# Kernel tuning notes

Measured on AMD Instinct MI355X. Metric: run time of the kernel, lower is better.

## Reference

```python
import jax, jax.numpy as jnp
import numpy as np

N_USER = 100_000
N_ITEM = 100_000
E = 1_600_000
D_IN = 128
H = 64
OUT = 2


def _lin_init(k, din, dout):
    kw, kb = jax.random.split(k)
    bound = 1.0 / np.sqrt(din)
    W = jax.random.uniform(kw, (din, dout), jnp.float32, -bound, bound)
    b = jax.random.uniform(kb, (dout,), jnp.float32, -bound, bound)
    return W, b


def setup_inputs() -> dict:
    key = jax.random.key(0)
    ks = jax.random.split(key, 12)
    inp = {
        "x_user": jax.random.normal(ks[0], (N_USER, D_IN), jnp.float32),
        "x_item": jax.random.normal(ks[1], (N_ITEM, D_IN), jnp.float32),
        "ei_user": jax.random.randint(ks[2], (2, E), 0, N_USER, jnp.int32),
        "ei_item": jax.random.randint(ks[3], (2, E), 0, N_ITEM, jnp.int32),
    }
    inp["W1_user"], inp["b1_user"] = _lin_init(ks[4], D_IN, H)
    inp["W1_item"], inp["b1_item"] = _lin_init(ks[5], D_IN, H)
    inp["W2_user"], inp["b2_user"] = _lin_init(ks[6], H, H)
    inp["W2_item"], inp["b2_item"] = _lin_init(ks[7], H, H)
    inp["Wl_user"], inp["bl_user"] = _lin_init(ks[8], H, OUT)
    inp["Wl_item"], inp["bl_item"] = _lin_init(ks[9], H, OUT)
    return inp


def gcn_conv(x, W, b, src, dst, n):
    # PyG GCNConv: h = x @ W; symmetric norm with added self-loops; scatter-add to dst; + bias
    loop = jnp.arange(n, dtype=src.dtype)
    s = jnp.concatenate([src, loop])  # [E+n]
    d = jnp.concatenate([dst, loop])
    deg = jax.ops.segment_sum(jnp.ones(s.shape[0], x.dtype), d, num_segments=n)
    dinv = jnp.where(deg > 0, jax.lax.rsqrt(deg), 0.0)
    norm = dinv[s] * dinv[d]  # [E+n]
    h = x @ W  # [n, out]
    msg = h[s] * norm[:, None]  # gather + scale, [E+n, out]
    return jax.ops.segment_sum(msg, d, num_segments=n) + b


def reference(x_user, x_item, ei_user, ei_item,
              W1_user, b1_user, W1_item, b1_item,
              W2_user, b2_user, W2_item, b2_item,
              Wl_user, bl_user, Wl_item, bl_item):
    # layer 1 (HeteroConv with one GCNConv per node type's relation) + relu; dropout = identity (eval)
    h_u = jax.nn.relu(gcn_conv(x_user, W1_user, b1_user, ei_user[0], ei_user[1], N_USER))
    h_i = jax.nn.relu(gcn_conv(x_item, W1_item, b1_item, ei_item[0], ei_item[1], N_ITEM))
    # layer 2 + relu
    h_u = jax.nn.relu(gcn_conv(h_u, W2_user, b2_user, ei_user[0], ei_user[1], N_USER))
    h_i = jax.nn.relu(gcn_conv(h_i, W2_item, b2_item, ei_item[0], ei_item[1], N_ITEM))
    # per-node-type output heads
    return (h_u @ Wl_user + bl_user, h_i @ Wl_item + bl_item)
```

## Files before the change

### kernel.cpp

```cpp
#include <hip/hip_runtime.h>

#define CDIV(a,b) (((a)+(b)-1)/(b))
#define NPB 256
#define PCHUNK 2048

typedef __attribute__((ext_vector_type(8))) short bf16x8;
typedef __attribute__((ext_vector_type(8))) unsigned short u16x8;
typedef __attribute__((ext_vector_type(4))) float f32x4;

__device__ __forceinline__ unsigned short f2bf(float x){
    unsigned int u = __float_as_uint(x);
    unsigned int r = u + 0x7FFFu + ((u >> 16) & 1u);
    return (unsigned short)(r >> 16);
}
__device__ __forceinline__ float bf2f(unsigned short h){
    return __uint_as_float(((unsigned int)h) << 16);
}

__global__ __launch_bounds__(256) void hg_wsplit_all(const float* __restrict__ W1u, const float* __restrict__ W1i,
                                                     const float* __restrict__ W2u, const float* __restrict__ W2i,
                                                     unsigned short* __restrict__ Bhi, unsigned short* __restrict__ Blo){
    const int sid = blockIdx.x*256 + threadIdx.x;
    if (sid >= 3072) return;
    const float* W; int slot, base;
    if (sid < 1024)      { W = W1u; slot = sid;        base = 0;     }
    else if (sid < 2048) { W = W1i; slot = sid - 1024; base = 8192;  }
    else if (sid < 2560) { W = W2u; slot = sid - 2048; base = 16384; }
    else                 { W = W2i; slot = sid - 2560; base = 20480; }
    const int l  = slot & 63;
    const int ct = (slot >> 6) & 3;
    const int ks = slot >> 8;
    const int kb = ks*32 + (l >> 4)*8;
    const int c  = ct*16 + (l & 15);
    #pragma unroll
    for (int j = 0; j < 8; ++j){
        const float w = W[(size_t)(kb + j)*64 + c];
        const unsigned short h = f2bf(w);
        Bhi[(size_t)base + (size_t)slot*8 + j] = h;
        Blo[(size_t)base + (size_t)slot*8 + j] = f2bf(w - bf2f(h));
    }
}

__device__ __forceinline__ void gemm1_body(int gb,
                                           const float* __restrict__ XU, const float* __restrict__ XI,
                                           const unsigned short* __restrict__ Bhi, const unsigned short* __restrict__ Blo,
                                           unsigned short* __restrict__ GU, unsigned short* __restrict__ GI,
                                           int NU, int NI, int gbU){
    const int type = (gb >= gbU);
    const int blk  = type ? gb - gbU : gb;
    const float* X = type ? XI : XU;
    unsigned short* G = type ? GI : GU;
    const int N    = type ? NI : NU;
    const unsigned short* Bh = Bhi + (type ? 8192 : 0);
    const unsigned short* Bl = Blo + (type ? 8192 : 0);

    const int l = threadIdx.x & 63;
    const int w = threadIdx.x >> 6;
    const int row0 = blk*64 + w*16;
    if (row0 >= N) return;

    f32x4 acc[4];
    #pragma unroll
    for (int ct = 0; ct < 4; ++ct) acc[ct] = (f32x4){0.f,0.f,0.f,0.f};

    const int rA = row0 + (l & 15);
    const int kg = (l >> 4) * 8;
    const bool rowok = (rA < N);
    const float* xrow = X + (size_t)rA * 128;

    #pragma unroll
    for (int ks = 0; ks < 4; ++ks){
        float xv[8];
        if (rowok){
            const float4 a = *(const float4*)(xrow + ks*32 + kg);
            const float4 b = *(const float4*)(xrow + ks*32 + kg + 4);
            xv[0]=a.x; xv[1]=a.y; xv[2]=a.z; xv[3]=a.w;
            xv[4]=b.x; xv[5]=b.y; xv[6]=b.z; xv[7]=b.w;
        } else {
            #pragma unroll
            for (int j = 0; j < 8; ++j) xv[j] = 0.f;
        }
        bf16x8 ahi, alo;
        #pragma unroll
        for (int j = 0; j < 8; ++j){
            const unsigned short h = f2bf(xv[j]);
            ahi[j] = (short)h;
            alo[j] = (short)f2bf(xv[j] - bf2f(h));
        }
        #pragma unroll
        for (int ct = 0; ct < 4; ++ct){
            const bf16x8 bhi = *(const bf16x8*)(Bh + ((size_t)(ks*4 + ct)*64 + l)*8);
            const bf16x8 blo = *(const bf16x8*)(Bl + ((size_t)(ks*4 + ct)*64 + l)*8);
            acc[ct] = __builtin_amdgcn_mfma_f32_16x16x32_bf16(ahi, bhi, acc[ct], 0, 0, 0);
            acc[ct] = __builtin_amdgcn_mfma_f32_16x16x32_bf16(alo, bhi, acc[ct], 0, 0, 0);
            acc[ct] = __builtin_amdgcn_mfma_f32_16x16x32_bf16(ahi, blo, acc[ct], 0, 0, 0);
        }
    }

    const int orow0 = row0 + (l >> 4)*4;
    const int ocol  = l & 15;
    #pragma unroll
    for (int r = 0; r < 4; ++r){
        const int orow = orow0 + r;
        if (orow < N){
            #pragma unroll
            for (int ct = 0; ct < 4; ++ct)
                G[(size_t)orow*64 + ct*16 + ocol] = f2bf(acc[ct][r]);
        }
    }
}

#define GEMM_TAIL(taskTot) \
    if ((int)blockIdx.x >= (taskTot)){ \
        gemm1_body(goff + blockIdx.x - (taskTot), XU, XI, Bhi, Blo, GU, GI, NU, NI, gbU); \
        return; \
    }

__global__ __launch_bounds__(256) void hg_mega_chist(const int* __restrict__ eiU, const int* __restrict__ eiI,
                                                     int* __restrict__ chU, int* __restrict__ chI,
                                                     int EU, int EI, int pbU, int pbTot, int NB,
                                                     const float* __restrict__ XU, const float* __restrict__ XI,
                                                     const unsigned short* __restrict__ Bhi, const unsigned short* __restrict__ Blo,
                                                     unsigned short* __restrict__ GU, unsigned short* __restrict__ GI,
                                                     int NU, int NI, int gbU, int goff){
    GEMM_TAIL(pbTot)
    extern __shared__ int sh[];
    const int type = ((int)blockIdx.x >= pbU);
    const int blk  = type ? blockIdx.x - pbU : blockIdx.x;
    const int E    = type ? EI : EU;
    const int* dst = (type ? eiI : eiU) + E;
    int* chist     = (type ? chI : chU) + (size_t)blk * NB;
    for (int i = threadIdx.x; i < NB; i += 256) sh[i] = 0;
    __syncthreads();
    const int e0 = blk * PCHUNK;
    const int eend = min(e0 + PCHUNK, E);
    for (int e = e0 + threadIdx.x; e < eend; e += 256)
        atomicAdd(&sh[dst[e] >> 8], 1);
    __syncthreads();
    for (int i = threadIdx.x; i < NB; i += 256)
        chist[i] = sh[i];
}

__global__ __launch_bounds__(256) void hg_mega_colscan(int* __restrict__ chU, int* __restrict__ chI,
                                                       int* __restrict__ bhU, int* __restrict__ bhI,
                                                       int pbU, int pbI, int NB,
                                                       const float* __restrict__ XU, const float* __restrict__ XI,
                                                       const unsigned short* __restrict__ Bhi, const unsigned short* __restrict__ Blo,
                                                       unsigned short* __restrict__ GU, unsigned short* __restrict__ GI,
                                                       int NU, int NI, int gbU, int goff){
    GEMM_TAIL(2*NB)
    __shared__ int sc[256];
    const int type = ((int)blockIdx.x >= NB);
    const int b    = type ? blockIdx.x - NB : blockIdx.x;
    int* chist     = type ? chI : chU;
    int* bh        = type ? bhI : bhU;
    const int nch  = type ? pbI : pbU;
    const int t = threadIdx.x;
    int carry = 0;
    for (int seg = 0; seg < nch; seg += 256){
        const int idx = seg + t;
        const int v = (idx < nch) ? chist[(size_t)idx*NB + b] : 0;
        sc[t] = v;
        __syncthreads();
        for (int off = 1; off < 256; off <<= 1){
            int x = 0;
            if (t >= off) x = sc[t-off];
            __syncthreads();
            if (t >= off) sc[t] += x;
            __syncthreads();
        }
        if (idx < nch) chist[(size_t)idx*NB + b] = carry + sc[t] - v;
        const int tot = sc[255];
        __syncthreads();
        carry += tot;
    }
    if (t == 0) bh[b] = carry;
}

__global__ __launch_bounds__(256) void hg_mega_bscan(const int* __restrict__ bhU, const int* __restrict__ bhI,
                                                     int* __restrict__ boffU, int* __restrict__ boffI,
                                                     int NB, int EU, int EI,
                                                     const float* __restrict__ XU, const float* __restrict__ XI,
                                                     const unsigned short* __restrict__ Bhi, const unsigned short* __restrict__ Blo,
                                                     unsigned short* __restrict__ GU, unsigned short* __restrict__ GI,
                                                     int NU, int NI, int gbU, int goff){
    GEMM_TAIL(2)
    __shared__ int sc[256];
    const int type = blockIdx.x;
    const int* bh = type ? bhI : bhU;
    int* boff     = type ? boffI : boffU;
    const int E   = type ? EI : EU;
    const int t = threadIdx.x;
    const int i0 = 2*t, i1 = 2*t + 1;
    const int c0 = (i0 < NB) ? bh[i0] : 0;
    const int c1 = (i1 < NB) ? bh[i1] : 0;
    const int s = c0 + c1;
    sc[t] = s;
    __syncthreads();
    for (int off = 1; off < 256; off <<= 1){
        int x = 0;
        if (t >= off) x = sc[t-off];
        __syncthreads();
        if (t >= off) sc[t] += x;
        __syncthreads();
    }
    const int excl = sc[t] - s;
    if (i0 < NB) boff[i0] = excl;
    if (i1 < NB) boff[i1] = excl + c0;
    if (t == 0) boff[NB] = E;
}

__global__ __launch_bounds__(256) void hg_mega_part(const int* __restrict__ eiU, const int* __restrict__ eiI,
                                                    const int* __restrict__ chU, const int* __restrict__ chI,
                                                    const int* __restrict__ boffU, const int* __restrict__ boffI,
                                                    unsigned int* __restrict__ bkU, unsigned int* __restrict__ bkI,
                                                    int EU, int EI, int pbU, int pbTot, int NB,
                                                    const float* __restrict__ XU, const float* __restrict__ XI,
                                                    const unsigned short* __restrict__ Bhi, const unsigned short* __restrict__ Blo,
                                                    unsigned short* __restrict__ GU, unsigned short* __restrict__ GI,
                                                    int NU, int NI, int gbU, int goff){
    GEMM_TAIL(pbTot)
    extern __shared__ int sh[];
    int* lofs  = sh;
    int* lcur  = lofs + NB;
    int* lbase = lcur + NB;
    int* sc    = lbase + NB;
    unsigned int* stage = (unsigned int*)(sc + 256);
    int* gaddr = (int*)(stage + PCHUNK);

    const int type = ((int)blockIdx.x >= pbU);
    const int blk  = type ? blockIdx.x - pbU : blockIdx.x;
    const int E    = type ? EI : EU;
    const int* src = type ? eiI : eiU;
    const int* dst = src + E;
    const int* chist = (type ? chI : chU) + (size_t)blk * NB;
    const int* boff  = type ? boffI : boffU;
    unsigned int* bucketed = type ? bkI : bkU;

    const int t  = threadIdx.x;
    const int e0 = blk * PCHUNK;
    const int eend = min(e0 + PCHUNK, E);
    const int cnt  = eend - e0;

    int se[8], de[8];
    for (int i = t; i < NB; i += 256) lofs[i] = 0;
    __syncthreads();
    const int eb = e0 + t*8;
    if (eb + 8 <= E){
        const int4 sa = *(const int4*)(src + eb);
        const int4 sb = *(const int4*)(src + eb + 4);
        const int4 da = *(const int4*)(dst + eb);
        const int4 db = *(const int4*)(dst + eb + 4);
        se[0]=sa.x; se[1]=sa.y; se[2]=sa.z; se[3]=sa.w;
        se[4]=sb.x; se[5]=sb.y; se[6]=sb.z; se[7]=sb.w;
        de[0]=da.x; de[1]=da.y; de[2]=da.z; de[3]=da.w;
        de[4]=db.x; de[5]=db.y; de[6]=db.z; de[7]=db.w;
    } else {
        #pragma unroll
        for (int j = 0; j < 8; ++j){
            const int e = eb + j;
            se[j] = (e < E) ? src[e] : -1;
            de[j] = (e < E) ? dst[e] : -1;
        }
    }
    #pragma unroll
    for (int j = 0; j < 8; ++j)
        if (de[j] >= 0) atomicAdd(&lofs[de[j] >> 8], 1);
    __syncthreads();

    const int i0 = 2*t, i1 = 2*t + 1;
    const int c0 = (i0 < NB) ? lofs[i0] : 0;
    const int c1 = (i1 < NB) ? lofs[i1] : 0;
    if (i0 < NB) lbase[i0] = boff[i0] + chist[i0];
    if (i1 < NB) lbase[i1] = boff[i1] + chist[i1];
    const int s = c0 + c1;
    sc[t] = s;
    __syncthreads();
    for (int off = 1; off < 256; off <<= 1){
        int x = 0;
        if (t >= off) x = sc[t-off];
        __syncthreads();
        if (t >= off) sc[t] += x;
        __syncthreads();
    }
    const int excl = sc[t] - s;
    __syncthreads();
    if (i0 < NB){ lofs[i0] = excl;      lcur[i0] = excl; }
    if (i1 < NB){ lofs[i1] = excl + c0; lcur[i1] = excl + c0; }
    __syncthreads();

    #pragma unroll
    for (int j = 0; j < 8; ++j){
        if (de[j] >= 0){
            const int b = de[j] >> 8;
            const int p = atomicAdd(&lcur[b], 1);
            stage[p] = (unsigned int)se[j] | ((unsigned int)(de[j] & 255) << 24);
            gaddr[p] = lbase[b] + (p - lofs[b]);
        }
    }
    __syncthreads();

    for (int i = t; i < cnt; i += 256)
        bucketed[gaddr[i]] = stage[i];
}

__global__ __launch_bounds__(256) void hg_mega_build(const unsigned int* __restrict__ bkU, const unsigned int* __restrict__ bkI,
                                                     const int* __restrict__ boffU, const int* __restrict__ boffI,
                                                     float* __restrict__ dinvU, float* __restrict__ dinvI,
                                                     int* __restrict__ rowptrU, int* __restrict__ rowptrI,
                                                     int* __restrict__ csrU, int* __restrict__ csrI,
                                                     int NU, int NI, int EU, int EI, int nbU, int nbTot,
                                                     const float* __restrict__ XU, const float* __restrict__ XI,
                                                     const unsigned short* __restrict__ Bhi, const unsigned short* __restrict__ Blo,
                                                     unsigned short* __restrict__ GU, unsigned short* __restrict__ GI,
                                                     int gbU, int goff){
    GEMM_TAIL(nbTot)
    __shared__ int hist[NPB];
    __shared__ int sc[NPB];
    __shared__ int cur[NPB];
    const int type = ((int)blockIdx.x >= nbU);
    const int b    = type ? blockIdx.x - nbU : blockIdx.x;
    const unsigned int* bucketed = type ? bkI : bkU;
    const int* boff = type ? boffI : boffU;
    float* dinv     = type ? dinvI : dinvU;
    int* rowptr     = type ? rowptrI : rowptrU;
    int* csr_src    = type ? csrI : csrU;
    const int N     = type ? NI : NU;
    const int E     = type ? EI : EU;

    const int t   = threadIdx.x;
    const int beg = boff[b], end = boff[b+1];
    hist[t] = 0;
    __syncthreads();
    for (int i = beg + t; i < end; i += 256)
        atomicAdd(&hist[bucketed[i] >> 24], 1);
    __syncthreads();
    const int d = hist[t];
    sc[t] = d;
    __syncthreads();
    for (int off = 1; off < 256; off <<= 1){
        int x = 0;
        if (t >= off) x = sc[t-off];
        __syncthreads();
        if (t >= off) sc[t] += x;
        __syncthreads();
    }
    const int excl = sc[t] - d;
    const int v = b*NPB + t;
    if (v < N){
        dinv[v]   = rsqrtf((float)(d + 1));
        rowptr[v] = beg + excl;
    }
    if (b == 0 && t == 0) rowptr[N] = E;
    cur[t] = beg + excl;
    __syncthreads();
    for (int i = beg + t; i < end; i += 256){
        const unsigned int w = bucketed[i];
        const int p = atomicAdd(&cur[w >> 24], 1);
        csr_src[p] = (int)(w & 0x00FFFFFFu);
    }
}

__global__ __launch_bounds__(256) void hg_gemm2(const float* __restrict__ XU, const float* __restrict__ XI,
                                                const unsigned short* __restrict__ Bhi, const unsigned short* __restrict__ Blo,
                                                unsigned short* __restrict__ GU, unsigned short* __restrict__ GI,
                                                int NU, int NI, int gbU){
    const int type = ((int)blockIdx.x >= gbU);
    const int blk  = type ? blockIdx.x - gbU : blockIdx.x;
    const float* X = type ? XI : XU;
    unsigned short* G = type ? GI : GU;
    const int N    = type ? NI : NU;
    const unsigned short* Bh = Bhi + (type ? 20480 : 16384);
    const unsigned short* Bl = Blo + (type ? 20480 : 16384);

    const int l = threadIdx.x & 63;
    const int w = threadIdx.x >> 6;
    const int row0 = blk*64 + w*16;
    if (row0 >= N) return;

    f32x4 acc[4];
    #pragma unroll
    for (int ct = 0; ct < 4; ++ct) acc[ct] = (f32x4){0.f,0.f,0.f,0.f};

    const int rA = row0 + (l & 15);
    const int kg = (l >> 4) * 8;
    const bool rowok = (rA < N);
    const float* xrow = X + (size_t)rA * 64;

    #pragma unroll
    for (int ks = 0; ks < 2; ++ks){
        float xv[8];
        if (rowok){
            const float4 a = *(const float4*)(xrow + ks*32 + kg);
            const float4 b = *(const float4*)(xrow + ks*32 + kg + 4);
            xv[0]=a.x; xv[1]=a.y; xv[2]=a.z; xv[3]=a.w;
            xv[4]=b.x; xv[5]=b.y; xv[6]=b.z; xv[7]=b.w;
        } else {
            #pragma unroll
            for (int j = 0; j < 8; ++j) xv[j] = 0.f;
        }
        bf16x8 ahi, alo;
        #pragma unroll
        for (int j = 0; j < 8; ++j){
            const unsigned short h = f2bf(xv[j]);
            ahi[j] = (short)h;
            alo[j] = (short)f2bf(xv[j] - bf2f(h));
        }
        #pragma unroll
        for (int ct = 0; ct < 4; ++ct){
            const bf16x8 bhi = *(const bf16x8*)(Bh + ((size_t)(ks*4 + ct)*64 + l)*8);
            const bf16x8 blo = *(const bf16x8*)(Bl + ((size_t)(ks*4 + ct)*64 + l)*8);
            acc[ct] = __builtin_amdgcn_mfma_f32_16x16x32_bf16(ahi, bhi, acc[ct], 0, 0, 0);
            acc[ct] = __builtin_amdgcn_mfma_f32_16x16x32_bf16(alo, bhi, acc[ct], 0, 0, 0);
            acc[ct] = __builtin_amdgcn_mfma_f32_16x16x32_bf16(ahi, blo, acc[ct], 0, 0, 0);
        }
    }

    const int orow0 = row0 + (l >> 4)*4;
    const int ocol  = l & 15;
    #pragma unroll
    for (int r = 0; r < 4; ++r){
        const int orow = orow0 + r;
        if (orow < N){
            #pragma unroll
            for (int ct = 0; ct < 4; ++ct)
                G[(size_t)orow*64 + ct*16 + ocol] = f2bf(acc[ct][r]);
        }
    }
}

template<bool HEAD>
__device__ __forceinline__ void agg_body(const unsigned short* __restrict__ g,
                                         const int* __restrict__ csr_src, const int* __restrict__ rowptr,
                                         const float* __restrict__ dinv, const float* __restrict__ b,
                                         const float* __restrict__ Wl, const float* __restrict__ bl,
                                         float* __restrict__ outp, int blk, int N){
    const int wave = (blk*256 + (int)threadIdx.x) >> 6;
    const int sub  = (threadIdx.x >> 3) & 7;
    const int c8   = (threadIdx.x & 7) << 3;
    const int v    = wave*8 + sub;
    const bool ok  = (v < N);

    int beg = 0, cnt = 0;
    float dvv = 0.f;
    if (ok){ beg = rowptr[v]; cnt = rowptr[v+1] - beg; dvv = dinv[v]; }

    float acc[8];
    #pragma unroll
    for (int j = 0; j < 8; ++j) acc[j] = 0.f;
    if (ok){
        const u16x8 s = *(const u16x8*)(g + (size_t)v*64 + c8);
        #pragma unroll
        for (int j = 0; j < 8; ++j) acc[j] = bf2f(s[j]) * dvv;
    }

    int i = 0;
    for (; i + 8 <= cnt; i += 8){
        const int s0 = csr_src[beg+i+0]; const int s1 = csr_src[beg+i+1];
        const int s2 = csr_src[beg+i+2]; const int s3 = csr_src[beg+i+3];
        const int s4 = csr_src[beg+i+4]; const int s5 = csr_src[beg+i+5];
        const int s6 = csr_src[beg+i+6]; const int s7 = csr_src[beg+i+7];
        const float dv0 = dinv[s0]; const float dv1 = dinv[s1];
        const float dv2 = dinv[s2]; const float dv3 = dinv[s3];
        const float dv4 = dinv[s4]; const float dv5 = dinv[s5];
        const float dv6 = dinv[s6]; const float dv7 = dinv[s7];
        const u16x8 x0 = *(const u16x8*)(g + (size_t)s0*64 + c8);
        const u16x8 x1 = *(const u16x8*)(g + (size_t)s1*64 + c8);
        const u16x8 x2 = *(const u16x8*)(g + (size_t)s2*64 + c8);
        const u16x8 x3 = *(const u16x8*)(g + (size_t)s3*64 + c8);
        const u16x8 x4 = *(const u16x8*)(g + (size_t)s4*64 + c8);
        const u16x8 x5 = *(const u16x8*)(g + (size_t)s5*64 + c8);
        const u16x8 x6 = *(const u16x8*)(g + (size_t)s6*64 + c8);
        const u16x8 x7 = *(const u16x8*)(g + (size_t)s7*64 + c8);
        #pragma unroll
        for (int j = 0; j < 8; ++j){
            float a = fmaf(bf2f(x0[j]), dv0, fmaf(bf2f(x1[j]), dv1, fmaf(bf2f(x2[j]), dv2, bf2f(x3[j]) * dv3)));
            float c = fmaf(bf2f(x4[j]), dv4, fmaf(bf2f(x5[j]), dv5, fmaf(bf2f(x6[j]), dv6, bf2f(x7[j]) * dv7)));
            acc[j] += a + c;
        }
    }
    for (; i + 4 <= cnt; i += 4){
        const int s0 = csr_src[beg+i+0]; const int s1 = csr_src[beg+i+1];
        const int s2 = csr_src[beg+i+2]; const int s3 = csr_src[beg+i+3];
        const float dv0 = dinv[s0]; const float dv1 = dinv[s1];
        const float dv2 = dinv[s2]; const float dv3 = dinv[s3];
        const u16x8 x0 = *(const u16x8*)(g + (size_t)s0*64 + c8);
        const u16x8 x1 = *(const u16x8*)(g + (size_t)s1*64 + c8);
        const u16x8 x2 = *(const u16x8*)(g + (size_t)s2*64 + c8);
        const u16x8 x3 = *(const u16x8*)(g + (size_t)s3*64 + c8);
        #pragma unroll
        for (int j = 0; j < 8; ++j)
            acc[j] += fmaf(bf2f(x0[j]), dv0, fmaf(bf2f(x1[j]), dv1, fmaf(bf2f(x2[j]), dv2, bf2f(x3[j]) * dv3)));
    }
    for (; i < cnt; ++i){
        const int s0 = csr_src[beg+i];
        const float dv0 = dinv[s0];
        const u16x8 x0 = *(const u16x8*)(g + (size_t)s0*64 + c8);
        #pragma unroll
        for (int j = 0; j < 8; ++j) acc[j] = fmaf(bf2f(x0[j]), dv0, acc[j]);
    }

    float r[8];
    {
        const float4 b0 = *(const float4*)(b + c8);
        const float4 b1 = *(const float4*)(b + c8 + 4);
        r[0] = fmaxf(fmaf(acc[0], dvv, b0.x), 0.f);
        r[1] = fmaxf(fmaf(acc[1], dvv, b0.y), 0.f);
        r[2] = fmaxf(fmaf(acc[2], dvv, b0.z), 0.f);
        r[3] = fmaxf(fmaf(acc[3], dvv, b0.w), 0.f);
        r[4] = fmaxf(fmaf(acc[4], dvv, b1.x), 0.f);
        r[5] = fmaxf(fmaf(acc[5], dvv, b1.y), 0.f);
        r[6] = fmaxf(fmaf(acc[6], dvv, b1.z), 0.f);
        r[7] = fmaxf(fmaf(acc[7], dvv, b1.w), 0.f);
    }

    if (!HEAD){
        if (ok){
            float4 r0 = {r[0], r[1], r[2], r[3]};
            float4 r1 = {r[4], r[5], r[6], r[7]};
            *(float4*)(outp + (size_t)v*64 + c8)     = r0;
            *(float4*)(outp + (size_t)v*64 + c8 + 4) = r1;
        }
    } else {
        float p0 = 0.f, p1 = 0.f;
        #pragma unroll
        for (int j = 0; j < 8; ++j){
            const float2 wl = *(const float2*)(Wl + (size_t)(c8 + j)*2);
            p0 = fmaf(r[j], wl.x, p0);
            p1 = fmaf(r[j], wl.y, p1);
        }
        p0 += __shfl_xor(p0, 1); p1 += __shfl_xor(p1, 1);
        p0 += __shfl_xor(p0, 2); p1 += __shfl_xor(p1, 2);
        p0 += __shfl_xor(p0, 4); p1 += __shfl_xor(p1, 4);
        if (ok && (threadIdx.x & 7) == 0){
            float2 o; o.x = p0 + bl[0]; o.y = p1 + bl[1];
            *(float2*)(outp + (size_t)v*2) = o;
        }
    }
}

__global__ __launch_bounds__(256) void hg_aggregate3(const unsigned short* __restrict__ gU, const unsigned short* __restrict__ gI,
                                                     const int* __restrict__ csrU, const int* __restrict__ csrI,
                                                     const int* __restrict__ rowptrU, const int* __restrict__ rowptrI,
                                                     const float* __restrict__ dinvU, const float* __restrict__ dinvI,
                                                     const float* __restrict__ bU, const float* __restrict__ bI,
                                                     float* __restrict__ outU, float* __restrict__ outI,
                                                     int NU, int NI, int nbU){
    const int type = ((int)blockIdx.x >= nbU);
    const int blk  = type ? blockIdx.x - nbU : blockIdx.x;
    agg_body<false>(type ? gI : gU, type ? csrI : csrU, type ? rowptrI : rowptrU,
                    type ? dinvI : dinvU, type ? bI : bU, nullptr, nullptr,
                    type ? outI : outU, blk, type ? NI : NU);
}

__global__ __launch_bounds__(256) void hg_agghead(const unsigned short* __restrict__ gU, const unsigned short* __restrict__ gI,
                                                  const int* __restrict__ csrU, const int* __restrict__ csrI,
                                                  const int* __restrict__ rowptrU, const int* __restrict__ rowptrI,
                                                  const float* __restrict__ dinvU, const float* __restrict__ dinvI,
                                                  const float* __restrict__ bU, const float* __restrict__ bI,
                                                  const float* __restrict__ WlU, const float* __restrict__ WlI,
                                                  const float* __restrict__ blU, const float* __restrict__ blI,
                                                  float* __restrict__ outU, float* __restrict__ outI,
                                                  int NU, int NI, int nbU){
    const int type = ((int)blockIdx.x >= nbU);
    const int blk  = type ? blockIdx.x - nbU : blockIdx.x;
    agg_body<true>(type ? gI : gU, type ? csrI : csrU, type ? rowptrI : rowptrU,
                   type ? dinvI : dinvU, type ? bI : bU,
                   type ? WlI : WlU, type ? blI : blU,
                   type ? outI : outU, blk, type ? NI : NU);
}

extern "C" void kernel_launch(void* const* d_in, const int* in_sizes, int n_in,
                              void* d_out, int out_size, void* d_ws, size_t ws_size,
                              hipStream_t stream) {
    const float* x_user = (const float*)d_in[0];
    const float* x_item = (const float*)d_in[1];
    const int*  ei_user = (const int*)d_in[2];
    const int*  ei_item = (const int*)d_in[3];
    const float* W1_user = (const float*)d_in[4];
    const float* b1_user = (const float*)d_in[5];
    const float* W1_item = (const float*)d_in[6];
    const float* b1_item = (const float*)d_in[7];
    const float* W2_user = (const float*)d_in[8];
    const float* b2_user = (const float*)d_in[9];
    const float* W2_item = (const float*)d_in[10];
    const float* b2_item = (const float*)d_in[11];
    const float* Wl_user = (const float*)d_in[12];
    const float* bl_user = (const float*)d_in[13];
    const float* Wl_item = (const float*)d_in[14];
    const float* bl_item = (const float*)d_in[15];

    const int NU = in_sizes[0] / 128;
    const int NI = in_sizes[1] / 128;
    const int EU = in_sizes[2] / 2;
    const int EI = in_sizes[3] / 2;
    const int NBU = CDIV(NU, NPB);
    const int NBI = CDIV(NI, NPB);
    const int NB  = (NBU > NBI) ? NBU : NBI;
    const int pbU = CDIV(EU, PCHUNK), pbI = CDIV(EI, PCHUNK);

    char* w = (char*)d_ws;
    float* hFU = (float*)w;                     w += (size_t)NU * 64 * sizeof(float);
    float* hFI = (float*)w;                     w += (size_t)NI * 64 * sizeof(float);
    unsigned short* GU = (unsigned short*)w;    w += (size_t)NU * 64 * sizeof(unsigned short);
    unsigned short* GI = (unsigned short*)w;    w += (size_t)NI * 64 * sizeof(unsigned short);
    float* dinvU = (float*)w;                   w += (size_t)NU * sizeof(float);
    float* dinvI = (float*)w;                   w += (size_t)NI * sizeof(float);
    int* rowptrU = (int*)w;                     w += ((size_t)NU + 1) * sizeof(int);
    int* rowptrI = (int*)w;                     w += ((size_t)NI + 1) * sizeof(int);
    int* csrU = (int*)w;                        w += (size_t)EU * sizeof(int);
    int* csrI = (int*)w;                        w += (size_t)EI * sizeof(int);
    unsigned int* bkU = (unsigned int*)w;       w += (size_t)EU * sizeof(int);
    unsigned int* bkI = (unsigned int*)w;       w += (size_t)EI * sizeof(int);
    int* chU = (int*)w;                         w += (size_t)pbU * NB * sizeof(int);
    int* chI = (int*)w;                         w += (size_t)pbI * NB * sizeof(int);
    int* bhU = (int*)w;                         w += (size_t)NB * sizeof(int);
    int* bhI = (int*)w;                         w += (size_t)NB * sizeof(int);
    int* boffU = (int*)w;                       w += ((size_t)NB + 1) * sizeof(int);
    int* boffI = (int*)w;                       w += ((size_t)NB + 1) * sizeof(int);
    unsigned short* Bhi = (unsigned short*)w;   w += (size_t)24576 * sizeof(unsigned short);
    unsigned short* Blo = (unsigned short*)w;   w += (size_t)24576 * sizeof(unsigned short);

    float* out  = (float*)d_out;
    float* outU = out;
    float* outI = out + (size_t)2 * NU;

    const int gbU = CDIV(NU, 64), gbI = CDIV(NI, 64);
    const int GB = gbU + gbI;
    const int q = GB / 5;
    const int c1 = q, c2 = q, c3 = q, c4 = q, c5 = GB - 4*q;

    hg_wsplit_all<<<12, 256, 0, stream>>>(W1_user, W1_item, W2_user, W2_item, Bhi, Blo);

    hg_mega_chist<<<pbU + pbI + c1, 256, NB*sizeof(int), stream>>>(
        ei_user, ei_item, chU, chI, EU, EI, pbU, pbU + pbI, NB,
        x_user, x_item, Bhi, Blo, GU, GI, NU, NI, gbU, 0);
    hg_mega_colscan<<<2*NB + c2, 256, 0, stream>>>(
        chU, chI, bhU, bhI, pbU, pbI, NB,
        x_user, x_item, Bhi, Blo, GU, GI, NU, NI, gbU, c1);
    hg_mega_bscan<<<2 + c3, 256, 0, stream>>>(
        bhU, bhI, boffU, boffI, NB, EU, EI,
        x_user, x_item, Bhi, Blo, GU, GI, NU, NI, gbU, c1 + c2);
    const size_t p5lds = (size_t)(3*NB + 256 + 2*PCHUNK) * sizeof(int);
    hg_mega_part<<<pbU + pbI + c4, 256, p5lds, stream>>>(
        ei_user, ei_item, chU, chI, boffU, boffI, bkU, bkI, EU, EI, pbU, pbU + pbI, NB,
        x_user, x_item, Bhi, Blo, GU, GI, NU, NI, gbU, c1 + c2 + c3);
    hg_mega_build<<<NBU + NBI + c5, 256, 0, stream>>>(
        bkU, bkI, boffU, boffI, dinvU, dinvI, rowptrU, rowptrI, csrU, csrI,
        NU, NI, EU, EI, NBU, NBU + NBI,
        x_user, x_item, Bhi, Blo, GU, GI, gbU, c1 + c2 + c3 + c4);

    const int abU = CDIV(NU, 32), abI = CDIV(NI, 32);
    hg_aggregate3<<<abU + abI, 256, 0, stream>>>(GU, GI, csrU, csrI, rowptrU, rowptrI,
                                                 dinvU, dinvI, b1_user, b1_item, hFU, hFI, NU, NI, abU);

    hg_gemm2<<<gbU + gbI, 256, 0, stream>>>(hFU, hFI, Bhi, Blo, GU, GI, NU, NI, gbU);

    hg_agghead<<<abU + abI, 256, 0, stream>>>(GU, GI, csrU, csrI, rowptrU, rowptrI,
                                              dinvU, dinvI, b2_user, b2_item,
                                              Wl_user, Wl_item, bl_user, bl_item,
                                              outU, outI, NU, NI, abU);
}
```

Measured before the change: 256.2 us.

## Fuse layer-1 aggregation with layer-2 GEMM through shared memory

```diff
diff --git a/kernel.cpp b/kernel.cpp
--- a/kernel.cpp
+++ b/kernel.cpp
@@ -361,91 +361,14 @@
     }
 }
 
-__global__ __launch_bounds__(256) void hg_gemm2(const float* __restrict__ XU, const float* __restrict__ XI,
-                                                const unsigned short* __restrict__ Bhi, const unsigned short* __restrict__ Blo,
-                                                unsigned short* __restrict__ GU, unsigned short* __restrict__ GI,
-                                                int NU, int NI, int gbU){
-    const int type = ((int)blockIdx.x >= gbU);
-    const int blk  = type ? blockIdx.x - gbU : blockIdx.x;
-    const float* X = type ? XI : XU;
-    unsigned short* G = type ? GI : GU;
-    const int N    = type ? NI : NU;
-    const unsigned short* Bh = Bhi + (type ? 20480 : 16384);
-    const unsigned short* Bl = Blo + (type ? 20480 : 16384);
-
-    const int l = threadIdx.x & 63;
-    const int w = threadIdx.x >> 6;
-    const int row0 = blk*64 + w*16;
-    if (row0 >= N) return;
-
-    f32x4 acc[4];
-    #pragma unroll
-    for (int ct = 0; ct < 4; ++ct) acc[ct] = (f32x4){0.f,0.f,0.f,0.f};
-
-    const int rA = row0 + (l & 15);
-    const int kg = (l >> 4) * 8;
-    const bool rowok = (rA < N);
-    const float* xrow = X + (size_t)rA * 64;
-
-    #pragma unroll
-    for (int ks = 0; ks < 2; ++ks){
-        float xv[8];
-        if (rowok){
-            const float4 a = *(const float4*)(xrow + ks*32 + kg);
-            const float4 b = *(const float4*)(xrow + ks*32 + kg + 4);
-            xv[0]=a.x; xv[1]=a.y; xv[2]=a.z; xv[3]=a.w;
-            xv[4]=b.x; xv[5]=b.y; xv[6]=b.z; xv[7]=b.w;
-        } else {
-            #pragma unroll
-            for (int j = 0; j < 8; ++j) xv[j] = 0.f;
-        }
-        bf16x8 ahi, alo;
-        #pragma unroll
-        for (int j = 0; j < 8; ++j){
-            const unsigned short h = f2bf(xv[j]);
-            ahi[j] = (short)h;
-            alo[j] = (short)f2bf(xv[j] - bf2f(h));
-        }
-        #pragma unroll
-        for (int ct = 0; ct < 4; ++ct){
-            const bf16x8 bhi = *(const bf16x8*)(Bh + ((size_t)(ks*4 + ct)*64 + l)*8);
-            const bf16x8 blo = *(const bf16x8*)(Bl + ((size_t)(ks*4 + ct)*64 + l)*8);
-            acc[ct] = __builtin_amdgcn_mfma_f32_16x16x32_bf16(ahi, bhi, acc[ct], 0, 0, 0);
-            acc[ct] = __builtin_amdgcn_mfma_f32_16x16x32_bf16(alo, bhi, acc[ct], 0, 0, 0);
-            acc[ct] = __builtin_amdgcn_mfma_f32_16x16x32_bf16(ahi, blo, acc[ct], 0, 0, 0);
-        }
-    }
-
-    const int orow0 = row0 + (l >> 4)*4;
-    const int ocol  = l & 15;
-    #pragma unroll
-    for (int r = 0; r < 4; ++r){
-        const int orow = orow0 + r;
-        if (orow < N){
-            #pragma unroll
-            for (int ct = 0; ct < 4; ++ct)
-                G[(size_t)orow*64 + ct*16 + ocol] = f2bf(acc[ct][r]);
-        }
-    }
-}
-
-template<bool HEAD>
-__device__ __forceinline__ void agg_body(const unsigned short* __restrict__ g,
-                                         const int* __restrict__ csr_src, const int* __restrict__ rowptr,
-                                         const float* __restrict__ dinv, const float* __restrict__ b,
-                                         const float* __restrict__ Wl, const float* __restrict__ bl,
-                                         float* __restrict__ outp, int blk, int N){
-    const int wave = (blk*256 + (int)threadIdx.x) >> 6;
-    const int sub  = (threadIdx.x >> 3) & 7;
-    const int c8   = (threadIdx.x & 7) << 3;
-    const int v    = wave*8 + sub;
-    const bool ok  = (v < N);
-
+__device__ __forceinline__ void gather_core(const unsigned short* __restrict__ g,
+                                            const int* __restrict__ csr_src, const int* __restrict__ rowptr,
+                                            const float* __restrict__ dinv, int v, int c8, bool ok,
+                                            float* acc, float& dvv){
     int beg = 0, cnt = 0;
-    float dvv = 0.f;
+    dvv = 0.f;
     if (ok){ beg = rowptr[v]; cnt = rowptr[v+1] - beg; dvv = dinv[v]; }
 
-    float acc[8];
     #pragma unroll
     for (int j = 0; j < 8; ++j) acc[j] = 0.f;
     if (ok){
@@ -499,6 +422,131 @@
         #pragma unroll
         for (int j = 0; j < 8; ++j) acc[j] = fmaf(bf2f(x0[j]), dv0, acc[j]);
     }
+}
+
+__global__ __launch_bounds__(256) void hg_agg_gemm2(const unsigned short* __restrict__ gU, const unsigned short* __restrict__ gI,
+                                                    const int* __restrict__ csrU, const int* __restrict__ csrI,
+                                                    const int* __restrict__ rowptrU, const int* __restrict__ rowptrI,
+                                                    const float* __restrict__ dinvU, const float* __restrict__ dinvI,
+                                                    const float* __restrict__ bU, const float* __restrict__ bI,
+                                                    const unsigned short* __restrict__ Bhi, const unsigned short* __restrict__ Blo,
+                                                    unsigned short* __restrict__ G2U, unsigned short* __restrict__ G2I,
+                                                    int NU, int NI, int nbU){
+    __shared__ float hrow[32*68];
+    const int type = ((int)blockIdx.x >= nbU);
+    const int blk  = type ? blockIdx.x - nbU : blockIdx.x;
+    const unsigned short* g = type ? gI : gU;
+    const int* csr_src = type ? csrI : csrU;
+    const int* rowptr  = type ? rowptrI : rowptrU;
+    const float* dinv  = type ? dinvI : dinvU;
+    const float* b     = type ? bI : bU;
+    unsigned short* G2 = type ? G2I : G2U;
+    const int N        = type ? NI : NU;
+    const unsigned short* Bh = Bhi + (type ? 20480 : 16384);
+    const unsigned short* Bl = Blo + (type ? 20480 : 16384);
+
+    const int t = threadIdx.x;
+    const int nodeLocal = t >> 3;
+    const int c8 = (t & 7) << 3;
+    const int v = blk*32 + nodeLocal;
+    const bool ok = (v < N);
+
+    float acc[8]; float dvv;
+    gather_core(g, csr_src, rowptr, dinv, v, c8, ok, acc, dvv);
+
+    {
+        const float4 b0 = *(const float4*)(b + c8);
+        const float4 b1 = *(const float4*)(b + c8 + 4);
+        float r0 = ok ? fmaxf(fmaf(acc[0], dvv, b0.x), 0.f) : 0.f;
+        float r1 = ok ? fmaxf(fmaf(acc[1], dvv, b0.y), 0.f) : 0.f;
+        float r2 = ok ? fmaxf(fmaf(acc[2], dvv, b0.z), 0.f) : 0.f;
+        float r3 = ok ? fmaxf(fmaf(acc[3], dvv, b0.w), 0.f) : 0.f;
+        float r4 = ok ? fmaxf(fmaf(acc[4], dvv, b1.x), 0.f) : 0.f;
+        float r5 = ok ? fmaxf(fmaf(acc[5], dvv, b1.y), 0.f) : 0.f;
+        float r6 = ok ? fmaxf(fmaf(acc[6], dvv, b1.z), 0.f) : 0.f;
+        float r7 = ok ? fmaxf(fmaf(acc[7], dvv, b1.w), 0.f) : 0.f;
+        float* hr = hrow + nodeLocal*68 + c8;
+        hr[0]=r0; hr[1]=r1; hr[2]=r2; hr[3]=r3; hr[4]=r4; hr[5]=r5; hr[6]=r6; hr[7]=r7;
+    }
+    __syncthreads();
+
+    const int l  = t & 63;
+    const int wv = t >> 6;
+    const int rbase  = (wv & 1) * 16;
+    const int ctbase = (wv >> 1) * 2;
+
+    f32x4 acc2[2];
+    acc2[0] = (f32x4){0.f,0.f,0.f,0.f};
+    acc2[1] = (f32x4){0.f,0.f,0.f,0.f};
+
+    const int arow = rbase + (l & 15);
+    const int kg   = (l >> 4) * 8;
+    #pragma unroll
+    for (int ks = 0; ks < 2; ++ks){
+        const float* hr = hrow + arow*68 + ks*32 + kg;
+        const float4 a = *(const float4*)(hr);
+        const float4 c = *(const float4*)(hr + 4);
+        float xv[8] = {a.x,a.y,a.z,a.w,c.x,c.y,c.z,c.w};
+        bf16x8 ahi, alo;
+        #pragma unroll
+        for (int j = 0; j < 8; ++j){
+            const unsigned short h = f2bf(xv[j]);
+            ahi[j] = (short)h;
+            alo[j] = (short)f2bf(xv[j] - bf2f(h));
+        }
+        #pragma unroll
+        for (int ct = 0; ct < 2; ++ct){
+            const int slot = (ks*4 + ctbase + ct)*64 + l;
+            const bf16x8 bhi = *(const bf16x8*)(Bh + (size_t)slot*8);
+            const bf16x8 blo = *(const bf16x8*)(Bl + (size_t)slot*8);
+            acc2[ct] = __builtin_amdgcn_mfma_f32_16x16x32_bf16(ahi, bhi, acc2[ct], 0, 0, 0);
+            acc2[ct] = __builtin_amdgcn_mfma_f32_16x16x32_bf16(alo, bhi, acc2[ct], 0, 0, 0);
+            acc2[ct] = __builtin_amdgcn_mfma_f32_16x16x32_bf16(ahi, blo, acc2[ct], 0, 0, 0);
+        }
+    }
+
+    const int orow0 = rbase + (l >> 4)*4;
+    const int ocol  = l & 15;
+    #pragma unroll
+    for (int r = 0; r < 4; ++r){
+        const int gv = blk*32 + orow0 + r;
+        if (gv < N){
+            #pragma unroll
+            for (int ct = 0; ct < 2; ++ct)
+                G2[(size_t)gv*64 + (ctbase + ct)*16 + ocol] = f2bf(acc2[ct][r]);
+        }
+    }
+}
+
+__global__ __launch_bounds__(256) void hg_agghead(const unsigned short* __restrict__ gU, const unsigned short* __restrict__ gI,
+                                                  const int* __restrict__ csrU, const int* __restrict__ csrI,
+                                                  const int* __restrict__ rowptrU, const int* __restrict__ rowptrI,
+                                                  const float* __restrict__ dinvU, const float* __restrict__ dinvI,
+                                                  const float* __restrict__ bU, const float* __restrict__ bI,
+                                                  const float* __restrict__ WlU, const float* __restrict__ WlI,
+                                                  const float* __restrict__ blU, const float* __restrict__ blI,
+                                                  float* __restrict__ outU, float* __restrict__ outI,
+                                                  int NU, int NI, int nbU){
+    const int type = ((int)blockIdx.x >= nbU);
+    const int blk  = type ? blockIdx.x - nbU : blockIdx.x;
+    const unsigned short* g = type ? gI : gU;
+    const int* csr_src = type ? csrI : csrU;
+    const int* rowptr  = type ? rowptrI : rowptrU;
+    const float* dinv  = type ? dinvI : dinvU;
+    const float* b     = type ? bI : bU;
+    const float* Wl    = type ? WlI : WlU;
+    const float* bl    = type ? blI : blU;
+    float* outp        = type ? outI : outU;
+    const int N        = type ? NI : NU;
+
+    const int t = threadIdx.x;
+    const int nodeLocal = t >> 3;
+    const int c8 = (t & 7) << 3;
+    const int v = blk*32 + nodeLocal;
+    const bool ok = (v < N);
+
+    float acc[8]; float dvv;
+    gather_core(g, csr_src, rowptr, dinv, v, c8, ok, acc, dvv);
 
     float r[8];
     {
@@ -514,60 +562,20 @@
         r[7] = fmaxf(fmaf(acc[7], dvv, b1.w), 0.f);
     }
 
-    if (!HEAD){
-        if (ok){
-            float4 r0 = {r[0], r[1], r[2], r[3]};
-            float4 r1 = {r[4], r[5], r[6], r[7]};
-            *(float4*)(outp + (size_t)v*64 + c8)     = r0;
-            *(float4*)(outp + (size_t)v*64 + c8 + 4) = r1;
-        }
-    } else {
-        float p0 = 0.f, p1 = 0.f;
-        #pragma unroll
-        for (int j = 0; j < 8; ++j){
-            const float2 wl = *(const float2*)(Wl + (size_t)(c8 + j)*2);
-            p0 = fmaf(r[j], wl.x, p0);
-            p1 = fmaf(r[j], wl.y, p1);
-        }
-        p0 += __shfl_xor(p0, 1); p1 += __shfl_xor(p1, 1);
-        p0 += __shfl_xor(p0, 2); p1 += __shfl_xor(p1, 2);
-        p0 += __shfl_xor(p0, 4); p1 += __shfl_xor(p1, 4);
-        if (ok && (threadIdx.x & 7) == 0){
-            float2 o; o.x = p0 + bl[0]; o.y = p1 + bl[1];
-            *(float2*)(outp + (size_t)v*2) = o;
-        }
-    }
-}
-
-__global__ __launch_bounds__(256) void hg_aggregate3(const unsigned short* __restrict__ gU, const unsigned short* __restrict__ gI,
-                                                     const int* __restrict__ csrU, const int* __restrict__ csrI,
-                                                     const int* __restrict__ rowptrU, const int* __restrict__ rowptrI,
-                                                     const float* __restrict__ dinvU, const float* __restrict__ dinvI,
-                                                     const float* __restrict__ bU, const float* __restrict__ bI,
-                                                     float* __restrict__ outU, float* __restrict__ outI,
-                                                     int NU, int NI, int nbU){
-    const int type = ((int)blockIdx.x >= nbU);
-    const int blk  = type ? blockIdx.x - nbU : blockIdx.x;
-    agg_body<false>(type ? gI : gU, type ? csrI : csrU, type ? rowptrI : rowptrU,
-                    type ? dinvI : dinvU, type ? bI : bU, nullptr, nullptr,
-                    type ? outI : outU, blk, type ? NI : NU);
-}
-
-__global__ __launch_bounds__(256) void hg_agghead(const unsigned short* __restrict__ gU, const unsigned short* __restrict__ gI,
-                                                  const int* __restrict__ csrU, const int* __restrict__ csrI,
-                                                  const int* __restrict__ rowptrU, const int* __restrict__ rowptrI,
-                                                  const float* __restrict__ dinvU, const float* __restrict__ dinvI,
-                                                  const float* __restrict__ bU, const float* __restrict__ bI,
-                                                  const float* __restrict__ WlU, const float* __restrict__ WlI,
-                                                  const float* __restrict__ blU, const float* __restrict__ blI,
-                                                  float* __restrict__ outU, float* __restrict__ outI,
-                                                  int NU, int NI, int nbU){
-    const int type = ((int)blockIdx.x >= nbU);
-    const int blk  = type ? blockIdx.x - nbU : blockIdx.x;
-    agg_body<true>(type ? gI : gU, type ? csrI : csrU, type ? rowptrI : rowptrU,
-                   type ? dinvI : dinvU, type ? bI : bU,
-                   type ? WlI : WlU, type ? blI : blU,
-                   type ? outI : outU, blk, type ? NI : NU);
+    float p0 = 0.f, p1 = 0.f;
+    #pragma unroll
+    for (int j = 0; j < 8; ++j){
+        const float2 wl = *(const float2*)(Wl + (size_t)(c8 + j)*2);
+        p0 = fmaf(r[j], wl.x, p0);
+        p1 = fmaf(r[j], wl.y, p1);
+    }
+    p0 += __shfl_xor(p0, 1); p1 += __shfl_xor(p1, 1);
+    p0 += __shfl_xor(p0, 2); p1 += __shfl_xor(p1, 2);
+    p0 += __shfl_xor(p0, 4); p1 += __shfl_xor(p1, 4);
+    if (ok && (t & 7) == 0){
+        float2 o; o.x = p0 + bl[0]; o.y = p1 + bl[1];
+        *(float2*)(outp + (size_t)v*2) = o;
+    }
 }
 
 extern "C" void kernel_launch(void* const* d_in, const int* in_sizes, int n_in,
@@ -600,10 +608,10 @@
     const int pbU = CDIV(EU, PCHUNK), pbI = CDIV(EI, PCHUNK);
 
     char* w = (char*)d_ws;
-    float* hFU = (float*)w;                     w += (size_t)NU * 64 * sizeof(float);
-    float* hFI = (float*)w;                     w += (size_t)NI * 64 * sizeof(float);
     unsigned short* GU = (unsigned short*)w;    w += (size_t)NU * 64 * sizeof(unsigned short);
     unsigned short* GI = (unsigned short*)w;    w += (size_t)NI * 64 * sizeof(unsigned short);
+    unsigned short* G2U = (unsigned short*)w;   w += (size_t)NU * 64 * sizeof(unsigned short);
+    unsigned short* G2I = (unsigned short*)w;   w += (size_t)NI * 64 * sizeof(unsigned short);
     float* dinvU = (float*)w;                   w += (size_t)NU * sizeof(float);
     float* dinvI = (float*)w;                   w += (size_t)NI * sizeof(float);
     int* rowptrU = (int*)w;                     w += ((size_t)NU + 1) * sizeof(int);
@@ -651,12 +659,11 @@
         x_user, x_item, Bhi, Blo, GU, GI, gbU, c1 + c2 + c3 + c4);
 
     const int abU = CDIV(NU, 32), abI = CDIV(NI, 32);
-    hg_aggregate3<<<abU + abI, 256, 0, stream>>>(GU, GI, csrU, csrI, rowptrU, rowptrI,
-                                                 dinvU, dinvI, b1_user, b1_item, hFU, hFI, NU, NI, abU);
-
-    hg_gemm2<<<gbU + gbI, 256, 0, stream>>>(hFU, hFI, Bhi, Blo, GU, GI, NU, NI, gbU);
-
-    hg_agghead<<<abU + abI, 256, 0, stream>>>(GU, GI, csrU, csrI, rowptrU, rowptrI,
+    hg_agg_gemm2<<<abU + abI, 256, 0, stream>>>(GU, GI, csrU, csrI, rowptrU, rowptrI,
+                                                dinvU, dinvI, b1_user, b1_item,
+                                                Bhi, Blo, G2U, G2I, NU, NI, abU);
+
+    hg_agghead<<<abU + abI, 256, 0, stream>>>(G2U, G2I, csrU, csrI, rowptrU, rowptrI,
                                               dinvU, dinvI, b2_user, b2_item,
                                               Wl_user, Wl_item, bl_user, bl_item,
                                               outU, outI, NU, NI, abU);
```

New measurement: 240.7 us. 1.06x faster.
